# Optimization experiments

Hardware: AMD Instinct MI355X
Metric: run time of the kernel (lower is better)

## Reference

```python
import jax, jax.numpy as jnp
import numpy as np

# state_composition -> (modality, length); slices are consecutive offsets into D_state
COMP = [("joint_pos", 64), ("joint_vel", 64), ("eef_pose", 32), ("force", 32)]
NUM_EMB = 32   # num_embodiments
HID = 512      # hidden_size
EMB = 1024     # embed_dim
B, T = 16, 32


def setup_inputs() -> dict:
    key = jax.random.key(0)
    ks = iter(jax.random.split(key, 64))
    D = sum(L for _, L in COMP)
    inp = {
        "state_btD": jax.random.normal(next(ks), (B, T, D), jnp.float32),
        "embodiment_id_bt1": jax.random.randint(next(ks), (B, T, 1), 0, NUM_EMB, dtype=jnp.int64),
    }
    for m, L in COMP:
        inp[f"W1_{m}"] = 0.02 * jax.random.normal(next(ks), (NUM_EMB, L, HID), jnp.float32)
        inp[f"b1_{m}"] = jnp.zeros((NUM_EMB, HID), jnp.float32)
        inp[f"W2_{m}"] = 0.02 * jax.random.normal(next(ks), (NUM_EMB, HID, EMB), jnp.float32)
        inp[f"b2_{m}"] = jnp.zeros((NUM_EMB, EMB), jnp.float32)
        inp[f"te_{m}"] = 0.02 * jax.random.normal(next(ks), (1, 1, EMB), jnp.float32)
    return inp


def _cat_mlp(x, cat, W1, b1, W2, b2):
    # x: (N, in_dim), cat: (N,) int ids. Mirrors CategorySpecificMLP:
    # per-token weight gather W[cat] then bmm (here einsum over the token axis).
    h = jax.nn.relu(jnp.einsum("ni,nih->nh", x, W1[cat]) + b1[cat])
    return jnp.einsum("nh,nhe->ne", h, W2[cat]) + b2[cat]


def reference(state_btD, embodiment_id_bt1,
              W1_joint_pos, b1_joint_pos, W2_joint_pos, b2_joint_pos, te_joint_pos,
              W1_joint_vel, b1_joint_vel, W2_joint_vel, b2_joint_vel, te_joint_vel,
              W1_eef_pose, b1_eef_pose, W2_eef_pose, b2_eef_pose, te_eef_pose,
              W1_force, b1_force, W2_force, b2_force, te_force):
    Bv, Tv, D = state_btD.shape
    # expand (B,1,1) -> (B,T,1) if needed, then flatten to per-token ids
    cat = jnp.broadcast_to(embodiment_id_bt1, (Bv, Tv, 1)).reshape(Bv * Tv)
    params = [
        (W1_joint_pos, b1_joint_pos, W2_joint_pos, b2_joint_pos, te_joint_pos),
        (W1_joint_vel, b1_joint_vel, W2_joint_vel, b2_joint_vel, te_joint_vel),
        (W1_eef_pose, b1_eef_pose, W2_eef_pose, b2_eef_pose, te_eef_pose),
        (W1_force, b1_force, W2_force, b2_force, te_force),
    ]
    toks = []
    off = 0
    for (m, L), (W1, b1, W2, b2, te) in zip(COMP, params):
        x = state_btD[..., off:off + L].reshape(Bv * Tv, L)
        off += L
        z = _cat_mlp(x, cat, W1, b1, W2, b2) + te.reshape(EMB)
        toks.append(z.reshape(Bv, Tv, 1, EMB))
    return jnp.concatenate(toks, axis=2)  # (B, T, M, embed_dim)
```

## Files before the change

kernel.cpp:

```cpp
#include <hip/hip_runtime.h>

#define NCAT 32
#define NTOK 512
#define HID  512
#define EMB  1024
#define DSTATE 192


__global__ __launch_bounds__(512) void bucket_kernel(
    const int* __restrict__ ids, int* __restrict__ cnt, int* __restrict__ nW,
    int* __restrict__ work1, int* __restrict__ work2, int* __restrict__ toklist)
{
    __shared__ int scnt[NCAT];
    const int tid = threadIdx.x;
    if (tid < NCAT) scnt[tid] = 0;
    __syncthreads();
    const int c = ids[tid];
    const int pos = atomicAdd(&scnt[c], 1);
    toklist[c * NTOK + pos] = tid;
    __syncthreads();
    if (tid == 0) {
        int n1 = 0, n2 = 0;
        for (int cc = 0; cc < NCAT; ++cc) {
            const int n = scnt[cc];
            cnt[cc] = n;
            for (int ch = 0; ch * 8 < n; ++ch)  work1[n1++] = cc | (ch << 8);
            for (int ch = 0; ch * 16 < n; ++ch) work2[n2++] = cc | (ch << 8);
        }
        nW[0] = n1; nW[1] = n2;
    }
}

__global__ __launch_bounds__(256, 4) void layer1_kernel(
    const float* __restrict__ state,
    const int* __restrict__ cnt, const int* __restrict__ toklist,
    const int* __restrict__ nW, const int* __restrict__ work1,
    const float* __restrict__ W1_0, const float* __restrict__ W1_1,
    const float* __restrict__ W1_2, const float* __restrict__ W1_3,
    const float* __restrict__ b1_0, const float* __restrict__ b1_1,
    const float* __restrict__ b1_2, const float* __restrict__ b1_3,
    float* __restrict__ H)
{
    const int slot = blockIdx.x, mod = blockIdx.y;
    if (slot >= nW[0]) return;
    const int ent = work1[slot];
    const int cat = ent & 255, chunk = ent >> 8;
    const int nC = cnt[cat];
    const int start = chunk * 8;
    int nThis = nC - start;
    if (nThis > 8) nThis = 8;
    const int tid = threadIdx.x;
    const int col = blockIdx.z * 256 + tid;

    const int L   = (mod < 2) ? 64 : 32;
    const int lf4 = L >> 2;
    const int lsh = (mod < 2) ? 4 : 3;
    const int off = (mod == 0) ? 0 : (mod == 1) ? 64 : (mod == 2) ? 128 : 160;

    __shared__ float sX[8 * 64];
    __shared__ int sTok[8];
    if (tid < 8) sTok[tid] = (tid < nThis) ? toklist[cat * NTOK + start + tid] : 0;
    __syncthreads();

    if (tid < (8 << lsh)) {
        const int t = tid >> lsh, e = tid & (lf4 - 1);
        float4 v = make_float4(0.f, 0.f, 0.f, 0.f);
        if (t < nThis)
            v = ((const float4*)(state + sTok[t] * DSTATE + off))[e];
        ((float4*)sX)[t * lf4 + e] = v;
    }
    __syncthreads();

    const float* W1 = (mod == 0) ? W1_0 : (mod == 1) ? W1_1 : (mod == 2) ? W1_2 : W1_3;
    const float* b1 = (mod == 0) ? b1_0 : (mod == 1) ? b1_1 : (mod == 2) ? b1_2 : b1_3;
    const float* Wcol = W1 + cat * L * HID + col;

    float acc[8];
#pragma unroll
    for (int t = 0; t < 8; ++t) acc[t] = 0.f;

#pragma unroll 4
    for (int k4 = 0; k4 < lf4; ++k4) {
        const float* p = Wcol + (k4 * 4) * HID;
        const float w0 = p[0];
        const float w1 = p[HID];
        const float w2 = p[2 * HID];
        const float w3 = p[3 * HID];
#pragma unroll
        for (int t = 0; t < 8; ++t) {
            const float4 x4 = ((const float4*)sX)[t * lf4 + k4];
            acc[t] += x4.x * w0 + x4.y * w1 + x4.z * w2 + x4.w * w3;
        }
    }

    const float b = b1[cat * HID + col];
#pragma unroll
    for (int t = 0; t < 8; ++t) {
        if (t >= nThis) break;
        float h = acc[t] + b;
        H[(sTok[t] * 4 + mod) * HID + col] = h > 0.f ? h : 0.f;
    }
}

__global__ __launch_bounds__(256, 4) void layer2_kernel(
    const int* __restrict__ cnt, const int* __restrict__ toklist,
    const int* __restrict__ nW, const int* __restrict__ work2,
    const float* __restrict__ H,
    const float* __restrict__ W2_0, const float* __restrict__ W2_1,
    const float* __restrict__ W2_2, const float* __restrict__ W2_3,
    const float* __restrict__ b2_0, const float* __restrict__ b2_1,
    const float* __restrict__ b2_2, const float* __restrict__ b2_3,
    const float* __restrict__ te_0, const float* __restrict__ te_1,
    const float* __restrict__ te_2, const float* __restrict__ te_3,
    float* __restrict__ out)
{
    const int slot = blockIdx.x, mod = blockIdx.y;
    if (slot >= nW[1]) return;
    const int ent = work2[slot];
    const int cat = ent & 255, chunk = ent >> 8;
    const int nC = cnt[cat];
    const int start = chunk * 16;
    int nThis = nC - start;
    if (nThis > 16) nThis = 16;
    const int tid = threadIdx.x;
    const int col = blockIdx.z * 256 + tid;

    __shared__ float sH[16 * 512];
    __shared__ int sTok[16];
    if (tid < 16) sTok[tid] = (tid < nThis) ? toklist[cat * NTOK + start + tid] : 0;
    __syncthreads();

    for (int idx = tid; idx < 16 * 128; idx += 256) {
        const int t = idx >> 7, e4 = idx & 127;
        float4 v = make_float4(0.f, 0.f, 0.f, 0.f);
        if (t < nThis)
            v = ((const float4*)(H + (sTok[t] * 4 + mod) * HID))[e4];
        ((float4*)sH)[idx] = v;
    }
    __syncthreads();

    const float* W2 = (mod == 0) ? W2_0 : (mod == 1) ? W2_1 : (mod == 2) ? W2_2 : W2_3;
    const float* b2 = (mod == 0) ? b2_0 : (mod == 1) ? b2_1 : (mod == 2) ? b2_2 : b2_3;
    const float* te = (mod == 0) ? te_0 : (mod == 1) ? te_1 : (mod == 2) ? te_2 : te_3;

    const float* Wcol = W2 + cat * (HID * EMB) + col;

    float acc[16];
#pragma unroll
    for (int t = 0; t < 16; ++t) acc[t] = 0.f;

#pragma unroll 4
    for (int k4 = 0; k4 < 128; ++k4) {
        const float* p = Wcol + (k4 * 4) * EMB;
        const float w0 = p[0];
        const float w1 = p[EMB];
        const float w2 = p[2 * EMB];
        const float w3 = p[3 * EMB];
#pragma unroll
        for (int t = 0; t < 16; ++t) {
            const float4 h4 = ((const float4*)sH)[t * 128 + k4];
            acc[t] += h4.x * w0 + h4.y * w1 + h4.z * w2 + h4.w * w3;
        }
    }

    const float b = b2[cat * EMB + col] + te[col];
#pragma unroll
    for (int t = 0; t < 16; ++t) {
        if (t >= nThis) break;
        out[(sTok[t] * 4 + mod) * EMB + col] = acc[t] + b;
    }
}

extern "C" void kernel_launch(void* const* d_in, const int* in_sizes, int n_in,
                              void* d_out, int out_size, void* d_ws, size_t ws_size,
                              hipStream_t stream) {
    const float* state = (const float*)d_in[0];
    const int*   ids   = (const int*)d_in[1];
    const float *W1[4], *b1[4], *W2[4], *b2[4], *te[4];
    for (int m = 0; m < 4; ++m) {
        W1[m] = (const float*)d_in[2 + 5 * m + 0];
        b1[m] = (const float*)d_in[2 + 5 * m + 1];
        W2[m] = (const float*)d_in[2 + 5 * m + 2];
        b2[m] = (const float*)d_in[2 + 5 * m + 3];
        te[m] = (const float*)d_in[2 + 5 * m + 4];
    }
    char* ws = (char*)d_ws;
    int*   cnt     = (int*)ws;
    int*   nW      = (int*)(ws + 128);
    int*   work1   = (int*)(ws + 256);
    int*   work2   = (int*)(ws + 640);
    int*   toklist = (int*)(ws + 1024);
    float* H       = (float*)(ws + 66560);
    float* out     = (float*)d_out;

    bucket_kernel<<<1, 512, 0, stream>>>(ids, cnt, nW, work1, work2, toklist);
    layer1_kernel<<<dim3(96, 4, 2), 256, 0, stream>>>(
        state, cnt, toklist, nW, work1,
        W1[0], W1[1], W1[2], W1[3],
        b1[0], b1[1], b1[2], b1[3], H);
    layer2_kernel<<<dim3(64, 4, 4), 256, 0, stream>>>(
        cnt, toklist, nW, work2, H,
        W2[0], W2[1], W2[2], W2[3],
        b2[0], b2[1], b2[2], b2[3],
        te[0], te[1], te[2], te[3], out);
}
```

Measured before the change: 374.4 us.

## Compute four output columns per thread with float4 weight loads in both layers

Each thread now computes a 4-wide column vector using float4 weight loads, so one block covers the full hidden/embed width. The column-split grid dimension goes away. Layer 2 chunks drop from 16 to 8 tokens per block, which roughly doubles the work entries and grid slots (96) to keep parallelism. This cuts the number of weight load instructions and shares each H/X shared-memory read across four columns. In exchange, layer 2 re-reads the weights more often because of the smaller token chunks, and register pressure per thread rises.

```diff
diff --git a/kernel.cpp b/kernel.cpp
--- a/kernel.cpp
+++ b/kernel.cpp
@@ -24,14 +24,37 @@
         for (int cc = 0; cc < NCAT; ++cc) {
             const int n = scnt[cc];
             cnt[cc] = n;
-            for (int ch = 0; ch * 8 < n; ++ch)  work1[n1++] = cc | (ch << 8);
-            for (int ch = 0; ch * 16 < n; ++ch) work2[n2++] = cc | (ch << 8);
+            for (int ch = 0; ch * 8 < n; ++ch) work1[n1++] = cc | (ch << 8);
+            for (int ch = 0; ch * 8 < n; ++ch) work2[n2++] = cc | (ch << 8);
         }
         nW[0] = n1; nW[1] = n2;
     }
 }
 
-__global__ __launch_bounds__(256, 4) void layer1_kernel(
+template <int LF4>
+__device__ __forceinline__ void l1_kloop(
+    const float* __restrict__ Wcol, const float* __restrict__ sX,
+    float4* __restrict__ acc)
+{
+#pragma unroll 4
+    for (int k4 = 0; k4 < LF4; ++k4) {
+        const float* p = Wcol + (k4 * 4) * HID;
+        const float4 w0 = *(const float4*)(p);
+        const float4 w1 = *(const float4*)(p + HID);
+        const float4 w2 = *(const float4*)(p + 2 * HID);
+        const float4 w3 = *(const float4*)(p + 3 * HID);
+#pragma unroll
+        for (int t = 0; t < 8; ++t) {
+            const float4 x4 = ((const float4*)sX)[t * LF4 + k4];
+            acc[t].x += x4.x * w0.x + x4.y * w1.x + x4.z * w2.x + x4.w * w3.x;
+            acc[t].y += x4.x * w0.y + x4.y * w1.y + x4.z * w2.y + x4.w * w3.y;
+            acc[t].z += x4.x * w0.z + x4.y * w1.z + x4.z * w2.z + x4.w * w3.z;
+            acc[t].w += x4.x * w0.w + x4.y * w1.w + x4.z * w2.w + x4.w * w3.w;
+        }
+    }
+}
+
+__global__ __launch_bounds__(128, 2) void layer1_kernel(
     const float* __restrict__ state,
     const int* __restrict__ cnt, const int* __restrict__ toklist,
     const int* __restrict__ nW, const int* __restrict__ work1,
@@ -50,12 +73,12 @@
     int nThis = nC - start;
     if (nThis > 8) nThis = 8;
     const int tid = threadIdx.x;
-    const int col = blockIdx.z * 256 + tid;
-
-    const int L   = (mod < 2) ? 64 : 32;
-    const int lf4 = L >> 2;
-    const int lsh = (mod < 2) ? 4 : 3;
-    const int off = (mod == 0) ? 0 : (mod == 1) ? 64 : (mod == 2) ? 128 : 160;
+    const int col = 4 * tid;
+
+    const int L    = (mod < 2) ? 64 : 32;
+    const int lsh  = (mod < 2) ? 4 : 3;
+    const int lf4  = 1 << lsh;
+    const int off  = (mod == 0) ? 0 : (mod == 1) ? 64 : (mod == 2) ? 128 : 160;
 
     __shared__ float sX[8 * 64];
     __shared__ int sTok[8];
@@ -75,34 +98,27 @@
     const float* b1 = (mod == 0) ? b1_0 : (mod == 1) ? b1_1 : (mod == 2) ? b1_2 : b1_3;
     const float* Wcol = W1 + cat * L * HID + col;
 
-    float acc[8];
-#pragma unroll
-    for (int t = 0; t < 8; ++t) acc[t] = 0.f;
-
-#pragma unroll 4
-    for (int k4 = 0; k4 < lf4; ++k4) {
-        const float* p = Wcol + (k4 * 4) * HID;
-        const float w0 = p[0];
-        const float w1 = p[HID];
-        const float w2 = p[2 * HID];
-        const float w3 = p[3 * HID];
-#pragma unroll
-        for (int t = 0; t < 8; ++t) {
-            const float4 x4 = ((const float4*)sX)[t * lf4 + k4];
-            acc[t] += x4.x * w0 + x4.y * w1 + x4.z * w2 + x4.w * w3;
-        }
-    }
-
-    const float b = b1[cat * HID + col];
+    float4 acc[8];
+#pragma unroll
+    for (int t = 0; t < 8; ++t) acc[t] = make_float4(0.f, 0.f, 0.f, 0.f);
+
+    if (mod < 2) l1_kloop<16>(Wcol, sX, acc);
+    else         l1_kloop<8>(Wcol, sX, acc);
+
+    const float4 b = *(const float4*)(b1 + cat * HID + col);
 #pragma unroll
     for (int t = 0; t < 8; ++t) {
         if (t >= nThis) break;
-        float h = acc[t] + b;
-        H[(sTok[t] * 4 + mod) * HID + col] = h > 0.f ? h : 0.f;
-    }
-}
-
-__global__ __launch_bounds__(256, 4) void layer2_kernel(
+        float4 h;
+        h.x = acc[t].x + b.x; h.x = h.x > 0.f ? h.x : 0.f;
+        h.y = acc[t].y + b.y; h.y = h.y > 0.f ? h.y : 0.f;
+        h.z = acc[t].z + b.z; h.z = h.z > 0.f ? h.z : 0.f;
+        h.w = acc[t].w + b.w; h.w = h.w > 0.f ? h.w : 0.f;
+        *(float4*)(H + (sTok[t] * 4 + mod) * HID + col) = h;
+    }
+}
+
+__global__ __launch_bounds__(256, 2) void layer2_kernel(
     const int* __restrict__ cnt, const int* __restrict__ toklist,
     const int* __restrict__ nW, const int* __restrict__ work2,
     const float* __restrict__ H,
@@ -119,18 +135,18 @@
     const int ent = work2[slot];
     const int cat = ent & 255, chunk = ent >> 8;
     const int nC = cnt[cat];
-    const int start = chunk * 16;
+    const int start = chunk * 8;
     int nThis = nC - start;
-    if (nThis > 16) nThis = 16;
+    if (nThis > 8) nThis = 8;
     const int tid = threadIdx.x;
-    const int col = blockIdx.z * 256 + tid;
-
-    __shared__ float sH[16 * 512];
-    __shared__ int sTok[16];
-    if (tid < 16) sTok[tid] = (tid < nThis) ? toklist[cat * NTOK + start + tid] : 0;
-    __syncthreads();
-
-    for (int idx = tid; idx < 16 * 128; idx += 256) {
+    const int col = 4 * tid;
+
+    __shared__ float sH[8 * 512];
+    __shared__ int sTok[8];
+    if (tid < 8) sTok[tid] = (tid < nThis) ? toklist[cat * NTOK + start + tid] : 0;
+    __syncthreads();
+
+    for (int idx = tid; idx < 8 * 128; idx += 256) {
         const int t = idx >> 7, e4 = idx & 127;
         float4 v = make_float4(0.f, 0.f, 0.f, 0.f);
         if (t < nThis)
@@ -145,29 +161,39 @@
 
     const float* Wcol = W2 + cat * (HID * EMB) + col;
 
-    float acc[16];
-#pragma unroll
-    for (int t = 0; t < 16; ++t) acc[t] = 0.f;
-
-#pragma unroll 4
+    float4 acc[8];
+#pragma unroll
+    for (int t = 0; t < 8; ++t) acc[t] = make_float4(0.f, 0.f, 0.f, 0.f);
+
+#pragma unroll 2
     for (int k4 = 0; k4 < 128; ++k4) {
         const float* p = Wcol + (k4 * 4) * EMB;
-        const float w0 = p[0];
-        const float w1 = p[EMB];
-        const float w2 = p[2 * EMB];
-        const float w3 = p[3 * EMB];
-#pragma unroll
-        for (int t = 0; t < 16; ++t) {
+        const float4 w0 = *(const float4*)(p);
+        const float4 w1 = *(const float4*)(p + EMB);
+        const float4 w2 = *(const float4*)(p + 2 * EMB);
+        const float4 w3 = *(const float4*)(p + 3 * EMB);
+#pragma unroll
+        for (int t = 0; t < 8; ++t) {
             const float4 h4 = ((const float4*)sH)[t * 128 + k4];
-            acc[t] += h4.x * w0 + h4.y * w1 + h4.z * w2 + h4.w * w3;
+            acc[t].x += h4.x * w0.x + h4.y * w1.x + h4.z * w2.x + h4.w * w3.x;
+            acc[t].y += h4.x * w0.y + h4.y * w1.y + h4.z * w2.y + h4.w * w3.y;
+            acc[t].z += h4.x * w0.z + h4.y * w1.z + h4.z * w2.z + h4.w * w3.z;
+            acc[t].w += h4.x * w0.w + h4.y * w1.w + h4.z * w2.w + h4.w * w3.w;
         }
     }
 
-    const float b = b2[cat * EMB + col] + te[col];
-#pragma unroll
-    for (int t = 0; t < 16; ++t) {
+    const float4 bb = *(const float4*)(b2 + cat * EMB + col);
+    const float4 tt = *(const float4*)(te + col);
+    const float4 b4 = make_float4(bb.x + tt.x, bb.y + tt.y, bb.z + tt.z, bb.w + tt.w);
+#pragma unroll
+    for (int t = 0; t < 8; ++t) {
         if (t >= nThis) break;
-        out[(sTok[t] * 4 + mod) * EMB + col] = acc[t] + b;
+        float4 o;
+        o.x = acc[t].x + b4.x;
+        o.y = acc[t].y + b4.y;
+        o.z = acc[t].z + b4.z;
+        o.w = acc[t].w + b4.w;
+        *(float4*)(out + (sTok[t] * 4 + mod) * EMB + col) = o;
     }
 }
 
@@ -194,11 +220,11 @@
     float* out     = (float*)d_out;
 
     bucket_kernel<<<1, 512, 0, stream>>>(ids, cnt, nW, work1, work2, toklist);
-    layer1_kernel<<<dim3(96, 4, 2), 256, 0, stream>>>(
+    layer1_kernel<<<dim3(96, 4), 128, 0, stream>>>(
         state, cnt, toklist, nW, work1,
         W1[0], W1[1], W1[2], W1[3],
         b1[0], b1[1], b1[2], b1[3], H);
-    layer2_kernel<<<dim3(64, 4, 4), 256, 0, stream>>>(
+    layer2_kernel<<<dim3(96, 4), 256, 0, stream>>>(
         cnt, toklist, nW, work2, H,
         W2[0], W2[1], W2[2], W2[3],
         b2[0], b2[1], b2[2], b2[3],
```

Measured after the change: 373.4 us. About the same (-0.3%).

## Register-tile two columns per thread with double-buffered weight loads in both layers

Applied to the files above, without the earlier changes.

Each thread now computes two adjacent output columns using float2 weight loads, with half as many threads per block (128). A shared templated k-loop double-buffers groups of eight weight rows in registers so global loads overlap the FMAs from shared memory. Layer 1 now uses 16-token chunks and shares one work list with layer 2. The aim is to hide weight-streaming latency and reuse each shared-memory activation read across two columns. The cost is fewer threads and higher register pressure per thread, which may reduce occupancy.

```diff
diff --git a/kernel.cpp b/kernel.cpp
--- a/kernel.cpp
+++ b/kernel.cpp
@@ -5,11 +5,12 @@
 #define HID  512
 #define EMB  1024
 #define DSTATE 192
+#define CHUNK 16
 
 
 __global__ __launch_bounds__(512) void bucket_kernel(
     const int* __restrict__ ids, int* __restrict__ cnt, int* __restrict__ nW,
-    int* __restrict__ work1, int* __restrict__ work2, int* __restrict__ toklist)
+    int* __restrict__ work, int* __restrict__ toklist)
 {
     __shared__ int scnt[NCAT];
     const int tid = threadIdx.x;
@@ -20,21 +21,59 @@
     toklist[c * NTOK + pos] = tid;
     __syncthreads();
     if (tid == 0) {
-        int n1 = 0, n2 = 0;
+        int n1 = 0;
         for (int cc = 0; cc < NCAT; ++cc) {
             const int n = scnt[cc];
             cnt[cc] = n;
-            for (int ch = 0; ch * 8 < n; ++ch)  work1[n1++] = cc | (ch << 8);
-            for (int ch = 0; ch * 16 < n; ++ch) work2[n2++] = cc | (ch << 8);
+            for (int ch = 0; ch * CHUNK < n; ++ch) work[n1++] = cc | (ch << 8);
         }
-        nW[0] = n1; nW[1] = n2;
-    }
-}
-
-__global__ __launch_bounds__(256, 4) void layer1_kernel(
+        nW[0] = n1;
+    }
+}
+
+template <int NG, int WS>
+__device__ __forceinline__ void mlp_kloop(
+    const float* __restrict__ Wcol, const float4* __restrict__ sV,
+    float2* __restrict__ acc)
+{
+    float2 wa[8], wb[8];
+
+    auto LOADW = [&](float2* w, int g) {
+        const float* p = Wcol + (size_t)g * 8 * WS;
+#pragma unroll
+        for (int r = 0; r < 8; ++r) w[r] = *(const float2*)(p + r * WS);
+    };
+    auto FMAG = [&](const float2* w, int g) {
+#pragma unroll
+        for (int k4 = 0; k4 < 2; ++k4) {
+#pragma unroll
+            for (int t = 0; t < 16; ++t) {
+                const float4 v = sV[t * (2 * NG) + g * 2 + k4];
+                acc[t].x += v.x * w[4*k4+0].x + v.y * w[4*k4+1].x
+                          + v.z * w[4*k4+2].x + v.w * w[4*k4+3].x;
+                acc[t].y += v.x * w[4*k4+0].y + v.y * w[4*k4+1].y
+                          + v.z * w[4*k4+2].y + v.w * w[4*k4+3].y;
+            }
+        }
+    };
+
+    LOADW(wa, 0);
+    LOADW(wb, 1);
+#pragma unroll 1
+    for (int g = 0; g < NG - 4; g += 2) {
+        FMAG(wa, g);     LOADW(wa, g + 2);
+        FMAG(wb, g + 1); LOADW(wb, g + 3);
+    }
+    FMAG(wa, NG - 4); LOADW(wa, NG - 2);
+    FMAG(wb, NG - 3); LOADW(wb, NG - 1);
+    FMAG(wa, NG - 2);
+    FMAG(wb, NG - 1);
+}
+
+__global__ __launch_bounds__(128, 2) void layer1_kernel(
     const float* __restrict__ state,
     const int* __restrict__ cnt, const int* __restrict__ toklist,
-    const int* __restrict__ nW, const int* __restrict__ work1,
+    const int* __restrict__ nW, const int* __restrict__ work,
     const float* __restrict__ W1_0, const float* __restrict__ W1_1,
     const float* __restrict__ W1_2, const float* __restrict__ W1_3,
     const float* __restrict__ b1_0, const float* __restrict__ b1_1,
@@ -43,68 +82,59 @@
 {
     const int slot = blockIdx.x, mod = blockIdx.y;
     if (slot >= nW[0]) return;
-    const int ent = work1[slot];
+    const int ent = work[slot];
     const int cat = ent & 255, chunk = ent >> 8;
     const int nC = cnt[cat];
-    const int start = chunk * 8;
+    const int start = chunk * CHUNK;
     int nThis = nC - start;
-    if (nThis > 8) nThis = 8;
+    if (nThis > CHUNK) nThis = CHUNK;
     const int tid = threadIdx.x;
-    const int col = blockIdx.z * 256 + tid;
+    const int col = blockIdx.z * 256 + 2 * tid;
 
     const int L   = (mod < 2) ? 64 : 32;
-    const int lf4 = L >> 2;
     const int lsh = (mod < 2) ? 4 : 3;
+    const int lf4 = 1 << lsh;
     const int off = (mod == 0) ? 0 : (mod == 1) ? 64 : (mod == 2) ? 128 : 160;
 
-    __shared__ float sX[8 * 64];
-    __shared__ int sTok[8];
-    if (tid < 8) sTok[tid] = (tid < nThis) ? toklist[cat * NTOK + start + tid] : 0;
-    __syncthreads();
-
-    if (tid < (8 << lsh)) {
-        const int t = tid >> lsh, e = tid & (lf4 - 1);
+    __shared__ float4 sX[16 * 16];
+    __shared__ int sTok[16];
+    if (tid < 16) sTok[tid] = (tid < nThis) ? toklist[cat * NTOK + start + tid] : 0;
+    __syncthreads();
+
+    for (int idx = tid; idx < (16 << lsh); idx += 128) {
+        const int t = idx >> lsh, e = idx & (lf4 - 1);
         float4 v = make_float4(0.f, 0.f, 0.f, 0.f);
         if (t < nThis)
             v = ((const float4*)(state + sTok[t] * DSTATE + off))[e];
-        ((float4*)sX)[t * lf4 + e] = v;
+        sX[t * lf4 + e] = v;
     }
     __syncthreads();
 
     const float* W1 = (mod == 0) ? W1_0 : (mod == 1) ? W1_1 : (mod == 2) ? W1_2 : W1_3;
     const float* b1 = (mod == 0) ? b1_0 : (mod == 1) ? b1_1 : (mod == 2) ? b1_2 : b1_3;
-    const float* Wcol = W1 + cat * L * HID + col;
-
-    float acc[8];
-#pragma unroll
-    for (int t = 0; t < 8; ++t) acc[t] = 0.f;
-
-#pragma unroll 4
-    for (int k4 = 0; k4 < lf4; ++k4) {
-        const float* p = Wcol + (k4 * 4) * HID;
-        const float w0 = p[0];
-        const float w1 = p[HID];
-        const float w2 = p[2 * HID];
-        const float w3 = p[3 * HID];
-#pragma unroll
-        for (int t = 0; t < 8; ++t) {
-            const float4 x4 = ((const float4*)sX)[t * lf4 + k4];
-            acc[t] += x4.x * w0 + x4.y * w1 + x4.z * w2 + x4.w * w3;
-        }
-    }
-
-    const float b = b1[cat * HID + col];
-#pragma unroll
-    for (int t = 0; t < 8; ++t) {
+    const float* Wcol = W1 + (size_t)cat * L * HID + col;
+
+    float2 acc[16];
+#pragma unroll
+    for (int t = 0; t < 16; ++t) acc[t] = make_float2(0.f, 0.f);
+
+    if (mod < 2) mlp_kloop<8, HID>(Wcol, sX, acc);
+    else         mlp_kloop<4, HID>(Wcol, sX, acc);
+
+    const float2 b = *(const float2*)(b1 + cat * HID + col);
+#pragma unroll
+    for (int t = 0; t < 16; ++t) {
         if (t >= nThis) break;
-        float h = acc[t] + b;
-        H[(sTok[t] * 4 + mod) * HID + col] = h > 0.f ? h : 0.f;
-    }
-}
-
-__global__ __launch_bounds__(256, 4) void layer2_kernel(
+        float2 h;
+        h.x = acc[t].x + b.x; h.x = h.x > 0.f ? h.x : 0.f;
+        h.y = acc[t].y + b.y; h.y = h.y > 0.f ? h.y : 0.f;
+        *(float2*)(H + (size_t)(sTok[t] * 4 + mod) * HID + col) = h;
+    }
+}
+
+__global__ __launch_bounds__(128, 2) void layer2_kernel(
     const int* __restrict__ cnt, const int* __restrict__ toklist,
-    const int* __restrict__ nW, const int* __restrict__ work2,
+    const int* __restrict__ nW, const int* __restrict__ work,
     const float* __restrict__ H,
     const float* __restrict__ W2_0, const float* __restrict__ W2_1,
     const float* __restrict__ W2_2, const float* __restrict__ W2_3,
@@ -115,27 +145,27 @@
     float* __restrict__ out)
 {
     const int slot = blockIdx.x, mod = blockIdx.y;
-    if (slot >= nW[1]) return;
-    const int ent = work2[slot];
+    if (slot >= nW[0]) return;
+    const int ent = work[slot];
     const int cat = ent & 255, chunk = ent >> 8;
     const int nC = cnt[cat];
-    const int start = chunk * 16;
+    const int start = chunk * CHUNK;
     int nThis = nC - start;
-    if (nThis > 16) nThis = 16;
+    if (nThis > CHUNK) nThis = CHUNK;
     const int tid = threadIdx.x;
-    const int col = blockIdx.z * 256 + tid;
-
-    __shared__ float sH[16 * 512];
+    const int col = blockIdx.z * 256 + 2 * tid;
+
+    __shared__ float4 sH[16 * 128];
     __shared__ int sTok[16];
     if (tid < 16) sTok[tid] = (tid < nThis) ? toklist[cat * NTOK + start + tid] : 0;
     __syncthreads();
 
-    for (int idx = tid; idx < 16 * 128; idx += 256) {
+    for (int idx = tid; idx < 16 * 128; idx += 128) {
         const int t = idx >> 7, e4 = idx & 127;
         float4 v = make_float4(0.f, 0.f, 0.f, 0.f);
         if (t < nThis)
-            v = ((const float4*)(H + (sTok[t] * 4 + mod) * HID))[e4];
-        ((float4*)sH)[idx] = v;
+            v = ((const float4*)(H + (size_t)(sTok[t] * 4 + mod) * HID))[e4];
+        sH[idx] = v;
     }
     __syncthreads();
 
@@ -143,31 +173,22 @@
     const float* b2 = (mod == 0) ? b2_0 : (mod == 1) ? b2_1 : (mod == 2) ? b2_2 : b2_3;
     const float* te = (mod == 0) ? te_0 : (mod == 1) ? te_1 : (mod == 2) ? te_2 : te_3;
 
-    const float* Wcol = W2 + cat * (HID * EMB) + col;
-
-    float acc[16];
-#pragma unroll
-    for (int t = 0; t < 16; ++t) acc[t] = 0.f;
-
-#pragma unroll 4
-    for (int k4 = 0; k4 < 128; ++k4) {
-        const float* p = Wcol + (k4 * 4) * EMB;
-        const float w0 = p[0];
-        const float w1 = p[EMB];
-        const float w2 = p[2 * EMB];
-        const float w3 = p[3 * EMB];
-#pragma unroll
-        for (int t = 0; t < 16; ++t) {
-            const float4 h4 = ((const float4*)sH)[t * 128 + k4];
-            acc[t] += h4.x * w0 + h4.y * w1 + h4.z * w2 + h4.w * w3;
-        }
-    }
-
-    const float b = b2[cat * EMB + col] + te[col];
+    const float* Wcol = W2 + (size_t)cat * HID * EMB + col;
+
+    float2 acc[16];
+#pragma unroll
+    for (int t = 0; t < 16; ++t) acc[t] = make_float2(0.f, 0.f);
+
+    mlp_kloop<64, EMB>(Wcol, sH, acc);
+
+    const float2 bb = *(const float2*)(b2 + cat * EMB + col);
+    const float2 tt = *(const float2*)(te + col);
+    const float2 b2v = make_float2(bb.x + tt.x, bb.y + tt.y);
 #pragma unroll
     for (int t = 0; t < 16; ++t) {
         if (t >= nThis) break;
-        out[(sTok[t] * 4 + mod) * EMB + col] = acc[t] + b;
+        *(float2*)(out + (size_t)(sTok[t] * 4 + mod) * EMB + col) =
+            make_float2(acc[t].x + b2v.x, acc[t].y + b2v.y);
     }
 }
 
@@ -187,19 +208,18 @@
     char* ws = (char*)d_ws;
     int*   cnt     = (int*)ws;
     int*   nW      = (int*)(ws + 128);
-    int*   work1   = (int*)(ws + 256);
-    int*   work2   = (int*)(ws + 640);
+    int*   work    = (int*)(ws + 256);
     int*   toklist = (int*)(ws + 1024);
     float* H       = (float*)(ws + 66560);
     float* out     = (float*)d_out;
 
-    bucket_kernel<<<1, 512, 0, stream>>>(ids, cnt, nW, work1, work2, toklist);
-    layer1_kernel<<<dim3(96, 4, 2), 256, 0, stream>>>(
-        state, cnt, toklist, nW, work1,
+    bucket_kernel<<<1, 512, 0, stream>>>(ids, cnt, nW, work, toklist);
+    layer1_kernel<<<dim3(64, 4, 2), 128, 0, stream>>>(
+        state, cnt, toklist, nW, work,
         W1[0], W1[1], W1[2], W1[3],
         b1[0], b1[1], b1[2], b1[3], H);
-    layer2_kernel<<<dim3(64, 4, 4), 256, 0, stream>>>(
-        cnt, toklist, nW, work2, H,
+    layer2_kernel<<<dim3(64, 4, 4), 128, 0, stream>>>(
+        cnt, toklist, nW, work, H,
         W2[0], W2[1], W2[2], W2[3],
         b2[0], b2[1], b2[2], b2[3],
         te[0], te[1], te[2], te[3], out);
```

New measurement: 743.3 us. 98.6% more time.
